# Performance work log

Measured on AMD Instinct MI355X. Metric: run time of the kernel, lower is better.

## Reference

```python
import jax, jax.numpy as jnp
import numpy as np

B, S, D, H = 2, 2048, 1024, 16
DK = D // H  # 64
THETA = 10000.0


def _rope_tables(max_seq_len, d_k, theta):
    dim_idx = jnp.arange(0, d_k // 2, dtype=jnp.float32)
    freqs = 1.0 / theta ** (2.0 * dim_idx / d_k)
    pos = jnp.arange(0, max_seq_len, dtype=jnp.float32)
    ang = jnp.outer(pos, freqs)  # [S, d_k//2]
    return jnp.sin(ang), jnp.cos(ang)


def setup_inputs() -> dict:
    key = jax.random.key(0)
    ks = jax.random.split(key, 5)
    scale = 0.02
    x = jax.random.normal(ks[0], (B, S, D), dtype=jnp.float32)
    w_q = jax.random.normal(ks[1], (D, D), dtype=jnp.float32) * scale
    w_k = jax.random.normal(ks[2], (D, D), dtype=jnp.float32) * scale
    w_v = jax.random.normal(ks[3], (D, D), dtype=jnp.float32) * scale
    w_o = jax.random.normal(ks[4], (D, D), dtype=jnp.float32) * scale
    sin_tab, cos_tab = _rope_tables(S, DK, THETA)
    token_positions = jnp.broadcast_to(jnp.arange(S, dtype=jnp.int32), (B, S))
    return {"x": x, "w_q": w_q, "w_k": w_k, "w_v": w_v, "w_o": w_o,
            "sin_tab": sin_tab, "cos_tab": cos_tab,
            "token_positions": token_positions}


def _apply_rope(t, sin, cos):
    # t: [B, H, S, DK]; sin/cos: [B, 1, S, DK//2]
    t_even = t[..., 0::2]
    t_odd = t[..., 1::2]
    r_even = cos * t_even - sin * t_odd
    r_odd = sin * t_even + cos * t_odd
    # re-interleave even/odd back into last dim
    out = jnp.stack([r_even, r_odd], axis=-1)  # [B,H,S,DK//2,2]
    return out.reshape(t.shape)


def reference(x, w_q, w_k, w_v, w_o, sin_tab, cos_tab, token_positions):
    b, s, d = x.shape
    q = (x @ w_q.T).reshape(b, s, H, DK).transpose(0, 2, 1, 3)  # [B,H,S,DK]
    k = (x @ w_k.T).reshape(b, s, H, DK).transpose(0, 2, 1, 3)
    v = (x @ w_v.T).reshape(b, s, H, DK).transpose(0, 2, 1, 3)

    sin = sin_tab[token_positions][:, None, :, :]  # [B,1,S,DK//2]
    cos = cos_tab[token_positions][:, None, :, :]
    q = _apply_rope(q, sin, cos)
    k = _apply_rope(k, sin, cos)

    scores = jnp.einsum('bhqd,bhkd->bhqk', q, k) / jnp.sqrt(jnp.float32(DK))
    causal = jnp.tril(jnp.ones((s, s), dtype=bool))  # keep lower triangle
    scores = jnp.where(causal, scores, -jnp.inf)
    probs = jax.nn.softmax(scores, axis=-1)
    attn = jnp.einsum('bhqk,bhkd->bhqd', probs, v)
    attn = attn.transpose(0, 2, 1, 3).reshape(b, s, d)
    return attn @ w_o.T
```

## Files before the change

kernel.cpp:

```cpp
#include <hip/hip_runtime.h>
#include <hip/hip_bf16.h>
#include <cstdint>

#define B_ 2
#define S_ 2048
#define D_ 1024
#define H_ 16
#define DK_ 64
#define HALF_ 32

typedef short bf16x8 __attribute__((ext_vector_type(8)));
typedef float f32x4  __attribute__((ext_vector_type(4)));
typedef unsigned int u32;

static __device__ __forceinline__ unsigned short bfbits(float f) {
    __hip_bfloat16 h = __float2bfloat16(f);
    unsigned short u; __builtin_memcpy(&u, &h, 2); return u;
}
static __device__ __forceinline__ unsigned pack2bf(float a, float b) {
    return (unsigned)bfbits(a) | ((unsigned)bfbits(b) << 16);
}

static __device__ __forceinline__ void gload_lds16(const void* g, void* l) {
    __builtin_amdgcn_global_load_lds(
        (const __attribute__((address_space(1))) u32*)(uintptr_t)g,
        (__attribute__((address_space(3))) u32*)(uintptr_t)l,
        16, 0, 0);
}

__global__ __launch_bounds__(256) void to_bf16_kernel(
    const float* __restrict__ x,
    const float* __restrict__ wq, const float* __restrict__ wk,
    const float* __restrict__ wv, const float* __restrict__ wo,
    const float* __restrict__ sin_tab, const float* __restrict__ cos_tab,
    __hip_bfloat16* __restrict__ xb,
    __hip_bfloat16* __restrict__ wqb, __hip_bfloat16* __restrict__ wkb,
    __hip_bfloat16* __restrict__ wvb, __hip_bfloat16* __restrict__ wob,
    float2* __restrict__ sctab)
{
    const int seg = blockIdx.y;
    if (seg == 8) {
        if (blockIdx.x >= 64) return;
        size_t i = ((size_t)blockIdx.x * 256 + threadIdx.x) * 4;
        float4 c = *reinterpret_cast<const float4*>(cos_tab + i);
        float4 s = *reinterpret_cast<const float4*>(sin_tab + i);
        float4* dst = reinterpret_cast<float4*>(sctab + i);
        dst[0] = make_float4(c.x, s.x, c.y, s.y);
        dst[1] = make_float4(c.z, s.z, c.w, s.w);
        return;
    }
    const float* src;
    __hip_bfloat16* dst;
    size_t off = 0;
    if (seg < 4)       { src = x;  dst = xb;  off = (size_t)seg << 20; }
    else if (seg == 4) { src = wq; dst = wqb; }
    else if (seg == 5) { src = wk; dst = wkb; }
    else if (seg == 6) { src = wv; dst = wvb; }
    else               { src = wo; dst = wob; }
    size_t i = off + ((size_t)blockIdx.x * 256 + threadIdx.x) * 4;
    float4 v = *reinterpret_cast<const float4*>(src + i);
    ushort4 u = make_ushort4(bfbits(v.x), bfbits(v.y), bfbits(v.z), bfbits(v.w));
    *reinterpret_cast<ushort4*>(dst + i) = u;
}

template<int MODE>
__global__ __launch_bounds__(256) void mfma_gemm_kernel(
    const __hip_bfloat16* __restrict__ A,
    const __hip_bfloat16* __restrict__ Wq, const __hip_bfloat16* __restrict__ Wk,
    const __hip_bfloat16* __restrict__ Wv,
    __hip_bfloat16* __restrict__ out_q, __hip_bfloat16* __restrict__ out_k,
    __hip_bfloat16* __restrict__ out_v,
    float* __restrict__ out_f32,
    const float2* __restrict__ sctab,
    const int* __restrict__ tpos)
{
    constexpr int K = 1024;
    const int which = (MODE == 0) ? blockIdx.z : 3;
    const __hip_bfloat16* __restrict__ W =
        (MODE == 1) ? Wq : (which == 0 ? Wq : which == 1 ? Wk : Wv);

    __shared__ __align__(16) unsigned char As[2][128 * 4 * 16];
    __shared__ __align__(16) unsigned char Bs[2][128 * 4 * 16];

    const int tid = threadIdx.x;
    const int wid = tid >> 6;
    const int l   = tid & 63;
    const int g   = l >> 4;
    const int i16 = l & 15;
    const int wr  = wid >> 1, wc = wid & 1;

    const int wg   = blockIdx.x;
    const int tile = (wg & 7) * 32 + (wg >> 3);
    const int row0 = (tile >> 3) * 128;
    const int col0 = (tile & 7) * 128;

    const __hip_bfloat16* Abase = A + (size_t)row0 * K;
    const __hip_bfloat16* Wbase = W + (size_t)col0 * K;

    f32x4 acc[4][4];
    const f32x4 zero = {0.f, 0.f, 0.f, 0.f};
    #pragma unroll
    for (int mi = 0; mi < 4; ++mi)
        #pragma unroll
        for (int ni = 0; ni < 4; ++ni) acc[mi][ni] = zero;

    int a_off[4], b_off[4];
    #pragma unroll
    for (int f = 0; f < 4; ++f) {
        int ra = wr * 64 + f * 16 + i16;
        a_off[f] = (ra * 4 + (g ^ ((ra >> 1) & 3))) * 16;
        int rb = wc * 64 + f * 16 + i16;
        b_off[f] = (rb * 4 + (g ^ ((rb >> 1) & 3))) * 16;
    }

    int st_goff[2], st_loff[2];
    #pragma unroll
    for (int it = 0; it < 2; ++it) {
        int c = it * 256 + wid * 64 + l;
        int row = c >> 2;
        int kc = (c & 3) ^ ((row >> 1) & 3);
        st_goff[it] = row * K + kc * 8;
        st_loff[it] = (it * 256 + wid * 64) * 16;
    }

    #pragma unroll
    for (int it = 0; it < 2; ++it) {
        gload_lds16(Abase + st_goff[it], &As[0][0] + st_loff[it]);
        gload_lds16(Wbase + st_goff[it], &Bs[0][0] + st_loff[it]);
    }
    __syncthreads();

    for (int t = 0; t < K / 32; ++t) {
        const int cur = t & 1;
        if (t + 1 < K / 32) {
            const int k1 = (t + 1) * 32;
            #pragma unroll
            for (int it = 0; it < 2; ++it) {
                gload_lds16(Abase + k1 + st_goff[it], &As[cur ^ 1][0] + st_loff[it]);
                gload_lds16(Wbase + k1 + st_goff[it], &Bs[cur ^ 1][0] + st_loff[it]);
            }
        }
        bf16x8 af[4], bfr[4];
        #pragma unroll
        for (int f = 0; f < 4; ++f) {
            af[f]  = *reinterpret_cast<const bf16x8*>(&As[cur][0] + a_off[f]);
            bfr[f] = *reinterpret_cast<const bf16x8*>(&Bs[cur][0] + b_off[f]);
        }
        #pragma unroll
        for (int mi = 0; mi < 4; ++mi)
            #pragma unroll
            for (int ni = 0; ni < 4; ++ni)
                acc[mi][ni] = __builtin_amdgcn_mfma_f32_16x16x32_bf16(
                    af[mi], bfr[ni], acc[mi][ni], 0, 0, 0);
        __syncthreads();
    }

    if (MODE == 0) {
        __hip_bfloat16* __restrict__ outp =
            which == 0 ? out_q : which == 1 ? out_k : out_v;
        const int head = (col0 >> 6) + wc;
        #pragma unroll
        for (int mi = 0; mi < 4; ++mi) {
            #pragma unroll
            for (int r = 0; r < 4; ++r) {
                const int gi = row0 + wr * 64 + mi * 16 + g * 4 + r;
                const int b_ = gi >> 11;
                const int s_ = gi & (S_ - 1);
                const int pos = tpos[gi];
                const float2* sc = sctab + pos * HALF_;
                __hip_bfloat16* orow =
                    outp + (((size_t)b_ * H_ + head) * S_ + s_) * DK_;
                #pragma unroll
                for (int ni = 0; ni < 4; ++ni) {
                    float val = acc[mi][ni][r];
                    float other = __shfl_xor(val, 1, 64);
                    const int dk = ni * 16 + i16;
                    float res;
                    if (which < 2) {
                        float2 cs = sc[ni * 8 + (i16 >> 1)];
                        res = (i16 & 1) ? fmaf(cs.y, other, cs.x * val)
                                        : (cs.x * val - cs.y * other);
                    } else {
                        res = val;
                    }
                    if (which == 0) res *= 0.180336880f;
                    orow[dk] = __float2bfloat16(res);
                }
            }
        }
    } else {
        #pragma unroll
        for (int mi = 0; mi < 4; ++mi) {
            #pragma unroll
            for (int r = 0; r < 4; ++r) {
                const int gi = row0 + wr * 64 + mi * 16 + g * 4 + r;
                float* orow = out_f32 + (size_t)gi * D_ + col0 + wc * 64;
                #pragma unroll
                for (int ni = 0; ni < 4; ++ni)
                    orow[ni * 16 + i16] = acc[mi][ni][r];
            }
        }
    }
}

__global__ __launch_bounds__(512) void flash_mfma_kernel(
    const __hip_bfloat16* __restrict__ q,
    const __hip_bfloat16* __restrict__ k,
    const __hip_bfloat16* __restrict__ v,
    __hip_bfloat16* __restrict__ attn)
{
    __shared__ __align__(16) unsigned char Ks[2][64 * 128];
    __shared__ __align__(16) unsigned char Vt[2][64 * 128];
    __shared__ __align__(16) unsigned char Ps[8][16 * 128];

    const int tid = threadIdx.x;
    const int w   = tid >> 6;
    const int l   = tid & 63;
    const int g   = l >> 4;
    const int i16 = l & 15;

    const int wgid = blockIdx.x;
    const int bh   = (wgid & 7) * 4 + ((wgid >> 3) & 3);
    const int qsb  = 15 - (wgid >> 5);

    const size_t base = (size_t)bh * S_ * DK_;
    const __hip_bfloat16* kb_ = k + base;
    const __hip_bfloat16* vb_ = v + base;

    const int ci     = w * 64 + l;
    const int krow   = ci >> 3;
    const int kchunk = (ci & 7) ^ (krow & 7);
    const int ksrc   = krow * DK_ + kchunk * 8;
    unsigned char* const pw = &Ps[w][0];

    const int qrow  = qsb * 128 + w * 16 + i16;
    const int qbase = qsb * 128 + w * 16;
    const int nt    = 2 * qsb + 2;

    bf16x8 qf0, qf1;
    {
        const __hip_bfloat16* qp = q + base + (size_t)qrow * DK_ + g * 8;
        qf0 = *reinterpret_cast<const bf16x8*>(qp);
        qf1 = *reinterpret_cast<const bf16x8*>(qp + 32);
    }

    f32x4 o[4] = {};
    float m_run = -1e30f, l_run = 0.0f;

    gload_lds16(kb_ + ksrc, &Ks[0][0] + w * 1024);
    {
        float4 vv = *reinterpret_cast<const float4*>(vb_ + l * DK_ + w * 8);
        const unsigned short* u = reinterpret_cast<const unsigned short*>(&vv);
        #pragma unroll
        for (int s = 0; s < 8; ++s) {
            int d = w * 8 + s;
            *reinterpret_cast<unsigned short*>(&Vt[0][0] + d * 128 +
                (((l >> 3) ^ (d & 7)) << 4) + (l & 7) * 2) = u[s];
        }
    }
    __syncthreads();

    for (int t = 0; t < nt; ++t) {
        const int cur = t & 1;
        const bool pre = (t + 1 < nt);
        float4 vv;
        if (pre) {
            gload_lds16(kb_ + (size_t)(t + 1) * 64 * DK_ + ksrc,
                        &Ks[cur ^ 1][0] + w * 1024);
            vv = *reinterpret_cast<const float4*>(
                vb_ + (size_t)(t + 1) * 64 * DK_ + l * DK_ + w * 8);
        }

        if (t * 64 <= qbase + 15) {
            f32x4 s_acc[4] = {};
            __builtin_amdgcn_s_setprio(1);
            #pragma unroll
            for (int jf = 0; jf < 4; ++jf) {
                int row = jf * 16 + i16;
                bf16x8 ak0 = *reinterpret_cast<const bf16x8*>(
                    &Ks[cur][0] + row * 128 + ((g ^ (row & 7)) << 4));
                s_acc[jf] = __builtin_amdgcn_mfma_f32_16x16x32_bf16(
                    ak0, qf0, s_acc[jf], 0, 0, 0);
                bf16x8 ak1 = *reinterpret_cast<const bf16x8*>(
                    &Ks[cur][0] + row * 128 + (((4 + g) ^ (row & 7)) << 4));
                s_acc[jf] = __builtin_amdgcn_mfma_f32_16x16x32_bf16(
                    ak1, qf1, s_acc[jf], 0, 0, 0);
            }
            __builtin_amdgcn_s_setprio(0);

            if (t * 64 + 63 > qbase) {
                #pragma unroll
                for (int jf = 0; jf < 4; ++jf)
                    #pragma unroll
                    for (int r = 0; r < 4; ++r)
                        if (t * 64 + jf * 16 + g * 4 + r > qrow)
                            s_acc[jf][r] = -1e30f;
            }

            float mx01 = fmaxf(fmaxf(s_acc[0][0], s_acc[0][1]),
                               fmaxf(s_acc[0][2], s_acc[0][3]));
            float mx02 = fmaxf(fmaxf(s_acc[1][0], s_acc[1][1]),
                               fmaxf(s_acc[1][2], s_acc[1][3]));
            float mx03 = fmaxf(fmaxf(s_acc[2][0], s_acc[2][1]),
                               fmaxf(s_acc[2][2], s_acc[2][3]));
            float mx04 = fmaxf(fmaxf(s_acc[3][0], s_acc[3][1]),
                               fmaxf(s_acc[3][2], s_acc[3][3]));
            float vmax = fmaxf(fmaxf(mx01, mx02), fmaxf(mx03, mx04));
            vmax = fmaxf(vmax, __shfl_xor(vmax, 16, 64));
            vmax = fmaxf(vmax, __shfl_xor(vmax, 32, 64));

            if (!__all(vmax <= m_run + 11.5f)) {
                float m_new = fmaxf(m_run, vmax);
                float factor = __builtin_amdgcn_exp2f(m_run - m_new);
                m_run = m_new;
                l_run *= factor;
                #pragma unroll
                for (int df = 0; df < 4; ++df)
                    #pragma unroll
                    for (int r = 0; r < 4; ++r)
                        o[df][r] *= factor;
            }

            float p[4][4];
            float psum = 0.0f;
            #pragma unroll
            for (int jf = 0; jf < 4; ++jf)
                #pragma unroll
                for (int r = 0; r < 4; ++r) {
                    p[jf][r] = __builtin_amdgcn_exp2f(s_acc[jf][r] - m_run);
                    psum += p[jf][r];
                }
            psum += __shfl_xor(psum, 16, 64);
            psum += __shfl_xor(psum, 32, 64);
            l_run += psum;

            #pragma unroll
            for (int jf = 0; jf < 4; ++jf)
                #pragma unroll
                for (int r0 = 0; r0 < 4; r0 += 2) {
                    unsigned pk = pack2bf(p[jf][r0], p[jf][r0 + 1]);
                    int jj = jf * 16 + g * 4 + r0;
                    *reinterpret_cast<unsigned*>(pw + i16 * 128 +
                        ((jj * 2) ^ ((i16 & 7) << 4))) = pk;
                }

            __builtin_amdgcn_s_setprio(1);
            #pragma unroll
            for (int jc = 0; jc < 2; ++jc) {
                bf16x8 bp = *reinterpret_cast<const bf16x8*>(pw + i16 * 128 +
                    (((jc * 4 + g) ^ (i16 & 7)) << 4));
                #pragma unroll
                for (int df = 0; df < 4; ++df) {
                    int row = df * 16 + i16;
                    bf16x8 av = *reinterpret_cast<const bf16x8*>(
                        &Vt[cur][0] + row * 128 +
                        (((jc * 4 + g) ^ (row & 7)) << 4));
                    o[df] = __builtin_amdgcn_mfma_f32_16x16x32_bf16(
                        av, bp, o[df], 0, 0, 0);
                }
            }
            __builtin_amdgcn_s_setprio(0);
        }

        if (pre) {
            const unsigned short* u = reinterpret_cast<const unsigned short*>(&vv);
            unsigned char* vtb = &Vt[cur ^ 1][0];
            #pragma unroll
            for (int s = 0; s < 8; ++s) {
                int d = w * 8 + s;
                *reinterpret_cast<unsigned short*>(vtb + d * 128 +
                    (((l >> 3) ^ (d & 7)) << 4) + (l & 7) * 2) = u[s];
            }
        }
        __syncthreads();
    }

    const float inv_l = 1.0f / l_run;
    const int b_ = bh >> 4, h_ = bh & 15;
    __hip_bfloat16* orow = attn + ((size_t)b_ * S_ + qrow) * D_ + h_ * 64;
    #pragma unroll
    for (int df = 0; df < 4; ++df) {
        ushort4 uo = make_ushort4(
            bfbits(o[df][0] * inv_l), bfbits(o[df][1] * inv_l),
            bfbits(o[df][2] * inv_l), bfbits(o[df][3] * inv_l));
        *reinterpret_cast<ushort4*>(orow + df * 16 + g * 4) = uo;
    }
}

extern "C" void kernel_launch(void* const* d_in, const int* in_sizes, int n_in,
                              void* d_out, int out_size, void* d_ws, size_t ws_size,
                              hipStream_t stream) {
    const float* x       = (const float*)d_in[0];
    const float* w_q     = (const float*)d_in[1];
    const float* w_k     = (const float*)d_in[2];
    const float* w_v     = (const float*)d_in[3];
    const float* w_o     = (const float*)d_in[4];
    const float* sin_tab = (const float*)d_in[5];
    const float* cos_tab = (const float*)d_in[6];
    const int*   tpos    = (const int*)d_in[7];
    float* out = (float*)d_out;

    const size_t nM  = (size_t)B_ * S_ * D_;
    const size_t nW  = (size_t)D_ * D_;
    __hip_bfloat16* xb   = (__hip_bfloat16*)d_ws;
    __hip_bfloat16* wqb  = xb  + nM;
    __hip_bfloat16* wkb  = wqb + nW;
    __hip_bfloat16* wvb  = wkb + nW;
    __hip_bfloat16* wob  = wvb + nW;
    __hip_bfloat16* q_ws = wob + nW;
    __hip_bfloat16* k_ws = q_ws + nM;
    __hip_bfloat16* v_ws = k_ws + nM;
    __hip_bfloat16* a_ws = v_ws + nM;
    float2*         sct  = (float2*)(a_ws + nM);

    to_bf16_kernel<<<dim3(1024, 9), 256, 0, stream>>>(
        x, w_q, w_k, w_v, w_o, sin_tab, cos_tab,
        xb, wqb, wkb, wvb, wob, sct);
    mfma_gemm_kernel<0><<<dim3(256, 1, 3), 256, 0, stream>>>(
        xb, wqb, wkb, wvb, q_ws, k_ws, v_ws, nullptr, sct, tpos);
    flash_mfma_kernel<<<512, 512, 0, stream>>>(
        q_ws, k_ws, v_ws, a_ws);
    mfma_gemm_kernel<1><<<dim3(256, 1, 1), 256, 0, stream>>>(
        a_ws, wob, nullptr, nullptr, nullptr, nullptr, nullptr, out,
        sct, tpos);
}
```

Before: 132.4 us.

## Shrink flash attention query block to 64 rows with 4-wave workgroups

The flash attention kernel now uses 64-query blocks and 256-thread workgroups, launching 1024 blocks instead of 512 with 128-query, 512-thread blocks. K/V tile loading is redistributed so each thread loads two chunks, and the per-wave causal skip test is replaced by masking only on the final diagonal tile. The aim is finer causal load balancing, less wasted work on partially masked tiles, and more resident workgroups per CU. In exchange, each K/V tile is reused by half as many query rows, which doubles tile loads and barrier count per query.

```diff
diff --git a/kernel.cpp b/kernel.cpp
--- a/kernel.cpp
+++ b/kernel.cpp
@@ -203,7 +203,7 @@
     }
 }
 
-__global__ __launch_bounds__(512) void flash_mfma_kernel(
+__global__ __launch_bounds__(256) void flash_mfma_kernel(
     const __hip_bfloat16* __restrict__ q,
     const __hip_bfloat16* __restrict__ k,
     const __hip_bfloat16* __restrict__ v,
@@ -211,7 +211,7 @@
 {
     __shared__ __align__(16) unsigned char Ks[2][64 * 128];
     __shared__ __align__(16) unsigned char Vt[2][64 * 128];
-    __shared__ __align__(16) unsigned char Ps[8][16 * 128];
+    __shared__ __align__(16) unsigned char Ps[4][16 * 128];
 
     const int tid = threadIdx.x;
     const int w   = tid >> 6;
@@ -220,22 +220,31 @@
     const int i16 = l & 15;
 
     const int wgid = blockIdx.x;
-    const int bh   = (wgid & 7) * 4 + ((wgid >> 3) & 3);
-    const int qsb  = 15 - (wgid >> 5);
+    const int xcd  = wgid & 7;
+    const int idx  = wgid >> 3;
+    const int bh   = xcd * 4 + (idx & 3);
+    const int qsb  = 31 - (idx >> 2);
 
     const size_t base = (size_t)bh * S_ * DK_;
     const __hip_bfloat16* kb_ = k + base;
     const __hip_bfloat16* vb_ = v + base;
-
-    const int ci     = w * 64 + l;
-    const int krow   = ci >> 3;
-    const int kchunk = (ci & 7) ^ (krow & 7);
-    const int ksrc   = krow * DK_ + kchunk * 8;
+    const int nt = qsb + 1;
+
+    int ksrc[2], kdst[2];
+    int vj[2], vd8[2];
+    #pragma unroll
+    for (int it = 0; it < 2; ++it) {
+        int c = it * 256 + tid;
+        int krow = c >> 3;
+        int kchunk = (c & 7) ^ (krow & 7);
+        ksrc[it] = krow * DK_ + kchunk * 8;
+        kdst[it] = c * 16;
+        vj[it]  = c >> 3;
+        vd8[it] = c & 7;
+    }
     unsigned char* const pw = &Ps[w][0];
 
-    const int qrow  = qsb * 128 + w * 16 + i16;
-    const int qbase = qsb * 128 + w * 16;
-    const int nt    = 2 * qsb + 2;
+    const int qrow = qsb * 64 + w * 16 + i16;
 
     bf16x8 qf0, qf1;
     {
@@ -247,15 +256,19 @@
     f32x4 o[4] = {};
     float m_run = -1e30f, l_run = 0.0f;
 
-    gload_lds16(kb_ + ksrc, &Ks[0][0] + w * 1024);
-    {
-        float4 vv = *reinterpret_cast<const float4*>(vb_ + l * DK_ + w * 8);
+    #pragma unroll
+    for (int it = 0; it < 2; ++it)
+        gload_lds16(kb_ + ksrc[it], &Ks[0][0] + kdst[it]);
+    #pragma unroll
+    for (int it = 0; it < 2; ++it) {
+        float4 vv = *reinterpret_cast<const float4*>(
+            vb_ + vj[it] * DK_ + vd8[it] * 8);
         const unsigned short* u = reinterpret_cast<const unsigned short*>(&vv);
         #pragma unroll
         for (int s = 0; s < 8; ++s) {
-            int d = w * 8 + s;
+            int d = vd8[it] * 8 + s;
             *reinterpret_cast<unsigned short*>(&Vt[0][0] + d * 128 +
-                (((l >> 3) ^ (d & 7)) << 4) + (l & 7) * 2) = u[s];
+                (((vj[it] >> 3) ^ (d & 7)) << 4) + (vj[it] & 7) * 2) = u[s];
         }
     }
     __syncthreads();
@@ -263,113 +276,117 @@
     for (int t = 0; t < nt; ++t) {
         const int cur = t & 1;
         const bool pre = (t + 1 < nt);
-        float4 vv;
+        float4 vv0, vv1;
         if (pre) {
-            gload_lds16(kb_ + (size_t)(t + 1) * 64 * DK_ + ksrc,
-                        &Ks[cur ^ 1][0] + w * 1024);
-            vv = *reinterpret_cast<const float4*>(
-                vb_ + (size_t)(t + 1) * 64 * DK_ + l * DK_ + w * 8);
-        }
-
-        if (t * 64 <= qbase + 15) {
-            f32x4 s_acc[4] = {};
-            __builtin_amdgcn_s_setprio(1);
-            #pragma unroll
-            for (int jf = 0; jf < 4; ++jf) {
-                int row = jf * 16 + i16;
-                bf16x8 ak0 = *reinterpret_cast<const bf16x8*>(
-                    &Ks[cur][0] + row * 128 + ((g ^ (row & 7)) << 4));
-                s_acc[jf] = __builtin_amdgcn_mfma_f32_16x16x32_bf16(
-                    ak0, qf0, s_acc[jf], 0, 0, 0);
-                bf16x8 ak1 = *reinterpret_cast<const bf16x8*>(
-                    &Ks[cur][0] + row * 128 + (((4 + g) ^ (row & 7)) << 4));
-                s_acc[jf] = __builtin_amdgcn_mfma_f32_16x16x32_bf16(
-                    ak1, qf1, s_acc[jf], 0, 0, 0);
-            }
-            __builtin_amdgcn_s_setprio(0);
-
-            if (t * 64 + 63 > qbase) {
-                #pragma unroll
-                for (int jf = 0; jf < 4; ++jf)
-                    #pragma unroll
-                    for (int r = 0; r < 4; ++r)
-                        if (t * 64 + jf * 16 + g * 4 + r > qrow)
-                            s_acc[jf][r] = -1e30f;
-            }
-
-            float mx01 = fmaxf(fmaxf(s_acc[0][0], s_acc[0][1]),
-                               fmaxf(s_acc[0][2], s_acc[0][3]));
-            float mx02 = fmaxf(fmaxf(s_acc[1][0], s_acc[1][1]),
-                               fmaxf(s_acc[1][2], s_acc[1][3]));
-            float mx03 = fmaxf(fmaxf(s_acc[2][0], s_acc[2][1]),
-                               fmaxf(s_acc[2][2], s_acc[2][3]));
-            float mx04 = fmaxf(fmaxf(s_acc[3][0], s_acc[3][1]),
-                               fmaxf(s_acc[3][2], s_acc[3][3]));
-            float vmax = fmaxf(fmaxf(mx01, mx02), fmaxf(mx03, mx04));
-            vmax = fmaxf(vmax, __shfl_xor(vmax, 16, 64));
-            vmax = fmaxf(vmax, __shfl_xor(vmax, 32, 64));
-
-            if (!__all(vmax <= m_run + 11.5f)) {
-                float m_new = fmaxf(m_run, vmax);
-                float factor = __builtin_amdgcn_exp2f(m_run - m_new);
-                m_run = m_new;
-                l_run *= factor;
-                #pragma unroll
-                for (int df = 0; df < 4; ++df)
-                    #pragma unroll
-                    for (int r = 0; r < 4; ++r)
-                        o[df][r] *= factor;
-            }
-
-            float p[4][4];
-            float psum = 0.0f;
+            const size_t toff = (size_t)(t + 1) * 64 * DK_;
+            #pragma unroll
+            for (int it = 0; it < 2; ++it)
+                gload_lds16(kb_ + toff + ksrc[it], &Ks[cur ^ 1][0] + kdst[it]);
+            vv0 = *reinterpret_cast<const float4*>(vb_ + toff + vj[0] * DK_ + vd8[0] * 8);
+            vv1 = *reinterpret_cast<const float4*>(vb_ + toff + vj[1] * DK_ + vd8[1] * 8);
+        }
+
+        f32x4 s_acc[4] = {};
+        __builtin_amdgcn_s_setprio(1);
+        #pragma unroll
+        for (int jf = 0; jf < 4; ++jf) {
+            int row = jf * 16 + i16;
+            bf16x8 ak0 = *reinterpret_cast<const bf16x8*>(
+                &Ks[cur][0] + row * 128 + ((g ^ (row & 7)) << 4));
+            s_acc[jf] = __builtin_amdgcn_mfma_f32_16x16x32_bf16(
+                ak0, qf0, s_acc[jf], 0, 0, 0);
+            bf16x8 ak1 = *reinterpret_cast<const bf16x8*>(
+                &Ks[cur][0] + row * 128 + (((4 + g) ^ (row & 7)) << 4));
+            s_acc[jf] = __builtin_amdgcn_mfma_f32_16x16x32_bf16(
+                ak1, qf1, s_acc[jf], 0, 0, 0);
+        }
+        __builtin_amdgcn_s_setprio(0);
+
+        if (t == nt - 1) {
             #pragma unroll
             for (int jf = 0; jf < 4; ++jf)
                 #pragma unroll
-                for (int r = 0; r < 4; ++r) {
-                    p[jf][r] = __builtin_amdgcn_exp2f(s_acc[jf][r] - m_run);
-                    psum += p[jf][r];
-                }
-            psum += __shfl_xor(psum, 16, 64);
-            psum += __shfl_xor(psum, 32, 64);
-            l_run += psum;
-
-            #pragma unroll
-            for (int jf = 0; jf < 4; ++jf)
+                for (int r = 0; r < 4; ++r)
+                    if (t * 64 + jf * 16 + g * 4 + r > qrow)
+                        s_acc[jf][r] = -1e30f;
+        }
+
+        float mx0 = fmaxf(fmaxf(s_acc[0][0], s_acc[0][1]),
+                          fmaxf(s_acc[0][2], s_acc[0][3]));
+        float mx1 = fmaxf(fmaxf(s_acc[1][0], s_acc[1][1]),
+                          fmaxf(s_acc[1][2], s_acc[1][3]));
+        float mx2 = fmaxf(fmaxf(s_acc[2][0], s_acc[2][1]),
+                          fmaxf(s_acc[2][2], s_acc[2][3]));
+        float mx3 = fmaxf(fmaxf(s_acc[3][0], s_acc[3][1]),
+                          fmaxf(s_acc[3][2], s_acc[3][3]));
+        float vmax = fmaxf(fmaxf(mx0, mx1), fmaxf(mx2, mx3));
+        vmax = fmaxf(vmax, __shfl_xor(vmax, 16, 64));
+        vmax = fmaxf(vmax, __shfl_xor(vmax, 32, 64));
+
+        if (!__all(vmax <= m_run + 11.5f)) {
+            float m_new = fmaxf(m_run, vmax);
+            float factor = __builtin_amdgcn_exp2f(m_run - m_new);
+            m_run = m_new;
+            l_run *= factor;
+            #pragma unroll
+            for (int df = 0; df < 4; ++df)
                 #pragma unroll
-                for (int r0 = 0; r0 < 4; r0 += 2) {
-                    unsigned pk = pack2bf(p[jf][r0], p[jf][r0 + 1]);
-                    int jj = jf * 16 + g * 4 + r0;
-                    *reinterpret_cast<unsigned*>(pw + i16 * 128 +
-                        ((jj * 2) ^ ((i16 & 7) << 4))) = pk;
-                }
-
-            __builtin_amdgcn_s_setprio(1);
-            #pragma unroll
-            for (int jc = 0; jc < 2; ++jc) {
-                bf16x8 bp = *reinterpret_cast<const bf16x8*>(pw + i16 * 128 +
-                    (((jc * 4 + g) ^ (i16 & 7)) << 4));
-                #pragma unroll
-                for (int df = 0; df < 4; ++df) {
-                    int row = df * 16 + i16;
-                    bf16x8 av = *reinterpret_cast<const bf16x8*>(
-                        &Vt[cur][0] + row * 128 +
-                        (((jc * 4 + g) ^ (row & 7)) << 4));
-                    o[df] = __builtin_amdgcn_mfma_f32_16x16x32_bf16(
-                        av, bp, o[df], 0, 0, 0);
-                }
-            }
-            __builtin_amdgcn_s_setprio(0);
-        }
+                for (int r = 0; r < 4; ++r)
+                    o[df][r] *= factor;
+        }
+
+        float p[4][4];
+        float psum = 0.0f;
+        #pragma unroll
+        for (int jf = 0; jf < 4; ++jf)
+            #pragma unroll
+            for (int r = 0; r < 4; ++r) {
+                p[jf][r] = __builtin_amdgcn_exp2f(s_acc[jf][r] - m_run);
+                psum += p[jf][r];
+            }
+        psum += __shfl_xor(psum, 16, 64);
+        psum += __shfl_xor(psum, 32, 64);
+        l_run += psum;
+
+        #pragma unroll
+        for (int jf = 0; jf < 4; ++jf)
+            #pragma unroll
+            for (int r0 = 0; r0 < 4; r0 += 2) {
+                unsigned pk = pack2bf(p[jf][r0], p[jf][r0 + 1]);
+                int jj = jf * 16 + g * 4 + r0;
+                *reinterpret_cast<unsigned*>(pw + i16 * 128 +
+                    ((jj * 2) ^ ((i16 & 7) << 4))) = pk;
+            }
+
+        __builtin_amdgcn_s_setprio(1);
+        #pragma unroll
+        for (int jc = 0; jc < 2; ++jc) {
+            bf16x8 bp = *reinterpret_cast<const bf16x8*>(pw + i16 * 128 +
+                (((jc * 4 + g) ^ (i16 & 7)) << 4));
+            #pragma unroll
+            for (int df = 0; df < 4; ++df) {
+                int row = df * 16 + i16;
+                bf16x8 av = *reinterpret_cast<const bf16x8*>(
+                    &Vt[cur][0] + row * 128 +
+                    (((jc * 4 + g) ^ (row & 7)) << 4));
+                o[df] = __builtin_amdgcn_mfma_f32_16x16x32_bf16(
+                    av, bp, o[df], 0, 0, 0);
+            }
+        }
+        __builtin_amdgcn_s_setprio(0);
 
         if (pre) {
-            const unsigned short* u = reinterpret_cast<const unsigned short*>(&vv);
             unsigned char* vtb = &Vt[cur ^ 1][0];
+            const unsigned short* u0 = reinterpret_cast<const unsigned short*>(&vv0);
+            const unsigned short* u1 = reinterpret_cast<const unsigned short*>(&vv1);
             #pragma unroll
             for (int s = 0; s < 8; ++s) {
-                int d = w * 8 + s;
-                *reinterpret_cast<unsigned short*>(vtb + d * 128 +
-                    (((l >> 3) ^ (d & 7)) << 4) + (l & 7) * 2) = u[s];
+                int d0 = vd8[0] * 8 + s;
+                *reinterpret_cast<unsigned short*>(vtb + d0 * 128 +
+                    (((vj[0] >> 3) ^ (d0 & 7)) << 4) + (vj[0] & 7) * 2) = u0[s];
+                int d1 = vd8[1] * 8 + s;
+                *reinterpret_cast<unsigned short*>(vtb + d1 * 128 +
+                    (((vj[1] >> 3) ^ (d1 & 7)) << 4) + (vj[1] & 7) * 2) = u1[s];
             }
         }
         __syncthreads();
@@ -418,7 +435,7 @@
         xb, wqb, wkb, wvb, wob, sct);
     mfma_gemm_kernel<0><<<dim3(256, 1, 3), 256, 0, stream>>>(
         xb, wqb, wkb, wvb, q_ws, k_ws, v_ws, nullptr, sct, tpos);
-    flash_mfma_kernel<<<512, 512, 0, stream>>>(
+    flash_mfma_kernel<<<1024, 256, 0, stream>>>(
         q_ws, k_ws, v_ws, a_ws);
     mfma_gemm_kernel<1><<<dim3(256, 1, 1), 256, 0, stream>>>(
         a_ws, wob, nullptr, nullptr, nullptr, nullptr, nullptr, out,
```

Result: slower. 144.7 us (+9.3%).
